# Kernel optimization log

Measured on AMD Instinct MI355X. Metric: run time of the kernel, lower is better.

Reference implementation:

```python
import jax, jax.numpy as jnp
import numpy as np

BS, D = 4096, 128
NUM_CLASSES = 512
K = 4          # opt.pk
MARGIN = 0.1   # opt.margin
NEG = -1e30    # sentinel for masked-out entries (finite to avoid inf*0 NaNs)


def setup_inputs() -> dict:
    key = jax.random.key(0)
    k1, k2 = jax.random.split(key)
    batch_reprs = jax.random.normal(k1, (BS, D), dtype=jnp.float32)
    batch_labels = jax.random.randint(k2, (BS,), 0, NUM_CLASSES, dtype=jnp.int64)
    return {"batch_reprs": batch_reprs, "batch_labels": batch_labels}


def _pairwise_dist(x, eps=1e-16):
    # Euclidean distance matrix, squared=False, with the usual zero-distance
    # masking trick for sqrt differentiability (as in the source repo's dist()).
    prod = x @ x.T                              # [B,B]
    sq = jnp.diagonal(prod)                     # [B]
    d2 = jnp.maximum(sq[:, None] + sq[None, :] - 2.0 * prod, 0.0)
    zero_mask = (d2 == 0.0).astype(x.dtype)
    d = jnp.sqrt(d2 + zero_mask * eps)
    return d * (1.0 - zero_mask)


def reference(batch_reprs, batch_labels):
    # class-match matrix: 1 where same class (includes self-match on diagonal)
    cls_match = (batch_labels[:, None] == batch_labels[None, :]).astype(jnp.float32)  # [B,B]

    sim_mat = -_pairwise_dist(batch_reprs)                      # use_similarity=False path
    simi_hat = sim_mat + (1.0 - cls_match) * MARGIN             # margin-shifted similarities

    # rank positions (1-based) under descending sort of simi_hat, per row
    orgp = jnp.argsort(-simi_hat, axis=1)                       # descending order indices
    rank = jnp.argsort(orgp, axis=1) + 1                        # [B,B] int ranks

    pos_nums = jnp.sum(cls_match, axis=1).astype(jnp.int32)     # n_+ per row (incl. self)
    ks = jnp.minimum(pos_nums, K + 1)                           # clamp(max=k+1)

    fp_mask = (cls_match < 1.0) & (rank <= ks[:, None])         # false positives in top-k
    fp_nums = jnp.sum(fp_mask, axis=1)                          # |N| per row, int
    fn_mask = (cls_match > 0.0) & (rank > ks[:, None])          # false negatives beyond k

    # per-row top-|N| of false-negative similarities, vectorized over rows
    fn_vals = jnp.where(fn_mask, simi_hat, NEG)
    fn_sorted = -jnp.sort(-fn_vals, axis=1)                     # descending
    col = jnp.arange(simi_hat.shape[1])[None, :]
    top_fn_sum = jnp.sum(jnp.where(col < fp_nums[:, None], fn_sorted, 0.0), axis=1)

    fp_sum = jnp.sum(jnp.where(fp_mask, simi_hat, 0.0), axis=1)

    # rows with fp_num == 0 contribute 0 in both terms, matching the python loop
    return jnp.sum(fp_sum - top_fn_sum)
```

## Files before the change

kernel.cpp:

```cpp
#include <hip/hip_runtime.h>
#include <math.h>

#define BS 4096
#define D 128
#define NC 512
#define NS 32
#define SC 128
#define MARGINF 0.1f
#define NEGV -1e30f
#define BIGD 1e30f
#define LSTR 12

typedef float f32x4 __attribute__((ext_vector_type(4)));
typedef short s16x8 __attribute__((ext_vector_type(8)));

__device__ __forceinline__ unsigned short f2bf(float f) {
    unsigned int u = __float_as_uint(f);
    unsigned int r = u + 0x7FFFu + ((u >> 16) & 1u);
    return (unsigned short)(r >> 16);
}

__device__ __forceinline__ void insV(float v, float (&V)[5]) {
    float w0 = fminf(V[0], v);
    float w1 = __builtin_amdgcn_fmed3f(V[0], V[1], v);
    float w2 = __builtin_amdgcn_fmed3f(V[1], V[2], v);
    float w3 = __builtin_amdgcn_fmed3f(V[2], V[3], v);
    float w4 = __builtin_amdgcn_fmed3f(V[3], V[4], v);
    V[0] = w0; V[1] = w1; V[2] = w2; V[3] = w3; V[4] = w4;
}

__device__ __forceinline__ void insDF(float v, int f, float (&V)[5], int (&F)[5]) {
#pragma unroll
    for (int t = 0; t < 5; ++t) {
        bool c = v > V[t];
        float tv = V[t]; int tf = F[t];
        V[t] = c ? v : tv; F[t] = c ? f : tf;
        v = c ? tv : v;    f = c ? tf : f;
    }
}

__global__ __launch_bounds__(256) void prep_kernel(
        const float* __restrict__ X, const int* __restrict__ labels,
        float* __restrict__ norms, int* __restrict__ counts,
        unsigned short* __restrict__ Xp) {
    __shared__ __align__(16) unsigned short sb[32 * 128];
    const int t = threadIdx.x, bx = blockIdx.x;
    const int row0 = bx * 32;

#pragma unroll
    for (int i = 0; i < 4; ++i) {
        int idx = i * 256 + t;
        int lr = idx >> 5, kq = idx & 31;
        float4 v = ((const float4*)X)[(size_t)row0 * 32 + idx];
        float acc = v.x * v.x + v.y * v.y + v.z * v.z + v.w * v.w;
#pragma unroll
        for (int off = 1; off < 32; off <<= 1) acc += __shfl_xor(acc, off);
        if (kq == 0) norms[row0 + lr] = acc;
        ushort4 hv = { f2bf(v.x), f2bf(v.y), f2bf(v.z), f2bf(v.w) };
        int chunk = (kq >> 1) ^ (lr & 7);
        *(ushort4*)((char*)sb + lr * 256 + (chunk << 4) + (kq & 1) * 8) = hv;
    }
    if (t < 32) atomicAdd(&counts[labels[row0 + t]], 1);
    __syncthreads();

#pragma unroll
    for (int i = 0; i < 2; ++i) {
        int u = i * 256 + t;
        int j = u >> 8, ug = u & 255;
        int ks = ug >> 6, l2 = ug & 63;
        int lr = j * 16 + (l2 & 15), q = l2 >> 4;
        int chunk = (ks * 4 + q) ^ (lr & 7);
        ulonglong2 d = *(const ulonglong2*)((const char*)sb + lr * 256 + (chunk << 4));
        *(ulonglong2*)((char*)Xp + (size_t)(bx * 2 + j) * 4096 + ks * 1024 + l2 * 16) = d;
    }
}

__global__ __launch_bounds__(256, 8) void main_kernel(
        const unsigned short* __restrict__ Xp, const int* __restrict__ labels,
        const float* __restrict__ norms, float* __restrict__ lists) {
    const int t = threadIdx.x, bx = blockIdx.x;
    const int slice = bx & (NS - 1);
    const int col0 = slice * SC;
    const int w = t >> 6, l = t & 63, rl = l & 15, q = l >> 4;
    const int gRow = (bx >> 5) * 4 + w;
    const int rowG = gRow * 16 + rl;
    const int lR = labels[rowG];
    const char* Pb = (const char*)Xp;

    s16x8 brow[4];
#pragma unroll
    for (int ks = 0; ks < 4; ++ks)
        brow[ks] = *(const s16x8*)(Pb + (size_t)gRow * 4096 + ks * 1024 + l * 16);

    f32x4 acc[8];
#pragma unroll
    for (int i = 0; i < 8; ++i) acc[i] = (f32x4){0.f, 0.f, 0.f, 0.f};

#pragma unroll
    for (int ks = 0; ks < 4; ++ks) {
        s16x8 af[8];
#pragma unroll
        for (int i = 0; i < 8; ++i)
            af[i] = *(const s16x8*)(Pb + (size_t)(slice * 8 + i) * 4096 + ks * 1024 + l * 16);
#pragma unroll
        for (int i = 0; i < 8; ++i)
            acc[i] = __builtin_amdgcn_mfma_f32_16x16x32_bf16(af[i], brow[ks], acc[i], 0, 0, 0);
    }

    float dV[5], sV[5];
#pragma unroll
    for (int i = 0; i < 5; ++i) { dV[i] = BIGD; sV[i] = BIGD; }

#pragma unroll
    for (int i = 0; i < 8; ++i) {
        f32x4 nc4 = *(const f32x4*)(norms + col0 + i * 16 + q * 4);
        int4  lc4 = *(const int4*)(labels + col0 + i * 16 + q * 4);
        int lcv[4] = {lc4.x, lc4.y, lc4.z, lc4.w};
#pragma unroll
        for (int e = 0; e < 4; ++e) {
            float v = fmaf(acc[i][e], -2.f, nc4[e]);
            bool same = (lcv[e] == lR);
            insV(same ? BIGD : v, dV);
            if (__any(same)) insV(same ? v : BIGD, sV);
        }
    }

#pragma unroll
    for (int off = 16; off <= 32; off <<= 1) {
        float bv[5];
#pragma unroll
        for (int i = 0; i < 5; ++i) bv[i] = __shfl_xor(dV[i], off);
#pragma unroll
        for (int i = 0; i < 5; ++i) insV(bv[i], dV);
#pragma unroll
        for (int i = 0; i < 5; ++i) bv[i] = __shfl_xor(sV[i], off);
#pragma unroll
        for (int i = 0; i < 5; ++i) insV(bv[i], sV);
    }

    if (q == 0) {
        float* Lp = lists + ((size_t)rowG * NS + slice) * LSTR;
        *(f32x4*)Lp       = (f32x4){dV[0], dV[1], dV[2], dV[3]};
        *(f32x4*)(Lp + 4) = (f32x4){dV[4], sV[4], 0.f, 0.f};
        *(f32x4*)(Lp + 8) = (f32x4){sV[0], sV[1], sV[2], sV[3]};
    }
}

__global__ __launch_bounds__(256) void merge_kernel(
        const float* __restrict__ lists, const int* __restrict__ counts,
        const int* __restrict__ labels, const float* __restrict__ norms,
        float* __restrict__ partials) {
    __shared__ float sh[256];
    const int t = threadIdx.x, bx = blockIdx.x;
    const int gid = bx * 256 + t;
    const int r = gid >> 3, part = gid & 7;
    const int half = part & 1, s8 = part >> 1;

    float V[5];
#pragma unroll
    for (int i = 0; i < 5; ++i) V[i] = BIGD;
#pragma unroll
    for (int s = 0; s < 8; ++s) {
        const float* rec = lists + (size_t)(r * NS + s8 * 8 + s) * LSTR + half * 8;
        f32x4 v4 = *(const f32x4*)rec;
        float v5 = rec[half ? -3 : 4];
        insV(v4.x, V); insV(v4.y, V); insV(v4.z, V); insV(v4.w, V); insV(v5, V);
    }
#pragma unroll
    for (int off = 2; off <= 4; off <<= 1) {
        float bv[5];
#pragma unroll
        for (int i = 0; i < 5; ++i) bv[i] = __shfl_xor(V[i], off);
#pragma unroll
        for (int i = 0; i < 5; ++i) insV(bv[i], V);
    }
    float oV[5];
#pragma unroll
    for (int i = 0; i < 5; ++i) oV[i] = __shfl_xor(V[i], 1);

    float res = 0.f;
    if (part == 0) {
        const float nR = norms[r];
        const int pos = counts[labels[r]];
        const int ks = (pos < 5) ? pos : 5;
        float dS[5], sS[5];
#pragma unroll
        for (int i = 0; i < 5; ++i) {
            float dv = V[i];  bool ok = dv < 1e29f;
            dS[i] = ok ? (-sqrtf(fmaxf(nR + dv, 0.f)) + MARGINF) : NEGV;
        }
#pragma unroll
        for (int i = 0; i < 5; ++i) {
            float sv = oV[i]; bool ok = sv < 1e29f;
            sS[i] = ok ? -sqrtf(fmaxf(nR + sv, 0.f)) : NEGV;
        }
        float mV[5]; int mF[5];
#pragma unroll
        for (int i = 0; i < 5; ++i) { mV[i] = dS[i]; mF[i] = 0; }
#pragma unroll
        for (int i = 0; i < 5; ++i) insDF(sS[i], 1, mV, mF);

        float fpsum = 0.f; int fpn = 0;
#pragma unroll
        for (int i = 0; i < 5; ++i)
            if (i < ks && mF[i] == 0) { fpsum += mV[i]; fpn++; }
        const int s0 = ks - fpn;
        float fnsum = 0.f;
#pragma unroll
        for (int i = 0; i < 5; ++i)
            if (i >= s0 && i < s0 + fpn) fnsum += sS[i];
        res = fpsum - fnsum;
    }
    sh[t] = res;
    __syncthreads();
    for (int s = 128; s > 0; s >>= 1) {
        if (t < s) sh[t] += sh[t + s];
        __syncthreads();
    }
    if (t == 0) partials[bx] = sh[0];
}

__global__ void reduce_kernel(const float* __restrict__ partials, float* __restrict__ out) {
    const int l = threadIdx.x;
    float v = partials[l] + partials[l + 64];
#pragma unroll
    for (int off = 1; off < 64; off <<= 1) v += __shfl_xor(v, off);
    if (l == 0) out[0] = v;
}

extern "C" void kernel_launch(void* const* d_in, const int* in_sizes, int n_in,
                              void* d_out, int out_size, void* d_ws, size_t ws_size,
                              hipStream_t stream) {
    const float* X      = (const float*)d_in[0];
    const int*   labels = (const int*)d_in[1];

    float* ws       = (float*)d_ws;
    float* norms    = ws;
    float* partials = ws + BS;
    int*   counts   = (int*)(ws + BS + 128);
    float* lists    = ws + BS + 128 + NC;
    unsigned short* Xp = (unsigned short*)(lists + (size_t)BS * NS * LSTR);

    hipMemsetAsync(counts, 0, NC * sizeof(int), stream);
    prep_kernel<<<BS / 32, 256, 0, stream>>>(X, labels, norms, counts, Xp);
    main_kernel<<<(BS / 64) * NS, 256, 0, stream>>>(Xp, labels, norms, lists);
    merge_kernel<<<(BS * 8) / 256, 256, 0, stream>>>(lists, counts, labels, norms, partials);
    reduce_kernel<<<1, 64, 0, stream>>>(partials, (float*)d_out);
}
```

Measured before the change: 45.00 us.

## Widen column slices, simplify merge, fold final reduction into merge via ticket

Each main_kernel block now walks 512 columns in four 128-column groups instead of handling a single 128-column slice. This cuts the grid fourfold and shrinks the per-row candidate list buffer from 32 slices to 8. The merge kernel now reads one 8-slice record per thread and merges both distance lists with shuffles. The separate reduce kernel is replaced by a last-block-done atomic ticket that sums the partials, removing one launch. The costs are fewer, longer blocks that may hide latency less well, and a serial 128-element sum run by a single thread.

```diff
diff --git a/kernel.cpp b/kernel.cpp
--- a/kernel.cpp
+++ b/kernel.cpp
@@ -4,8 +4,8 @@
 #define BS 4096
 #define D 128
 #define NC 512
-#define NS 32
-#define SC 128
+#define NS 8
+#define SC 512
 #define MARGINF 0.1f
 #define NEGV -1e30f
 #define BIGD 1e30f
@@ -82,7 +82,7 @@
     const int slice = bx & (NS - 1);
     const int col0 = slice * SC;
     const int w = t >> 6, l = t & 63, rl = l & 15, q = l >> 4;
-    const int gRow = (bx >> 5) * 4 + w;
+    const int gRow = (bx >> 3) * 4 + w;
     const int rowG = gRow * 16 + rl;
     const int lR = labels[rowG];
     const char* Pb = (const char*)Xp;
@@ -92,36 +92,39 @@
     for (int ks = 0; ks < 4; ++ks)
         brow[ks] = *(const s16x8*)(Pb + (size_t)gRow * 4096 + ks * 1024 + l * 16);
 
-    f32x4 acc[8];
-#pragma unroll
-    for (int i = 0; i < 8; ++i) acc[i] = (f32x4){0.f, 0.f, 0.f, 0.f};
-
-#pragma unroll
-    for (int ks = 0; ks < 4; ++ks) {
-        s16x8 af[8];
-#pragma unroll
-        for (int i = 0; i < 8; ++i)
-            af[i] = *(const s16x8*)(Pb + (size_t)(slice * 8 + i) * 4096 + ks * 1024 + l * 16);
-#pragma unroll
-        for (int i = 0; i < 8; ++i)
-            acc[i] = __builtin_amdgcn_mfma_f32_16x16x32_bf16(af[i], brow[ks], acc[i], 0, 0, 0);
-    }
-
     float dV[5], sV[5];
 #pragma unroll
     for (int i = 0; i < 5; ++i) { dV[i] = BIGD; sV[i] = BIGD; }
 
-#pragma unroll
-    for (int i = 0; i < 8; ++i) {
-        f32x4 nc4 = *(const f32x4*)(norms + col0 + i * 16 + q * 4);
-        int4  lc4 = *(const int4*)(labels + col0 + i * 16 + q * 4);
-        int lcv[4] = {lc4.x, lc4.y, lc4.z, lc4.w};
-#pragma unroll
-        for (int e = 0; e < 4; ++e) {
-            float v = fmaf(acc[i][e], -2.f, nc4[e]);
-            bool same = (lcv[e] == lR);
-            insV(same ? BIGD : v, dV);
-            if (__any(same)) insV(same ? v : BIGD, sV);
+#pragma unroll 1
+    for (int cg = 0; cg < 4; ++cg) {
+        f32x4 acc[8];
+#pragma unroll
+        for (int i = 0; i < 8; ++i) acc[i] = (f32x4){0.f, 0.f, 0.f, 0.f};
+
+#pragma unroll
+        for (int ks = 0; ks < 4; ++ks) {
+            s16x8 af[8];
+#pragma unroll
+            for (int i = 0; i < 8; ++i)
+                af[i] = *(const s16x8*)(Pb + (size_t)(slice * 32 + cg * 8 + i) * 4096 + ks * 1024 + l * 16);
+#pragma unroll
+            for (int i = 0; i < 8; ++i)
+                acc[i] = __builtin_amdgcn_mfma_f32_16x16x32_bf16(af[i], brow[ks], acc[i], 0, 0, 0);
+        }
+
+#pragma unroll
+        for (int i = 0; i < 8; ++i) {
+            f32x4 nc4 = *(const f32x4*)(norms + col0 + cg * 128 + i * 16 + q * 4);
+            int4  lc4 = *(const int4*)(labels + col0 + cg * 128 + i * 16 + q * 4);
+            int lcv[4] = {lc4.x, lc4.y, lc4.z, lc4.w};
+#pragma unroll
+            for (int e = 0; e < 4; ++e) {
+                float v = fmaf(acc[i][e], -2.f, nc4[e]);
+                bool same = (lcv[e] == lR);
+                insV(same ? BIGD : v, dV);
+                if (__any(same)) insV(same ? v : BIGD, sV);
+            }
         }
     }
 
@@ -149,34 +152,32 @@
 __global__ __launch_bounds__(256) void merge_kernel(
         const float* __restrict__ lists, const int* __restrict__ counts,
         const int* __restrict__ labels, const float* __restrict__ norms,
-        float* __restrict__ partials) {
+        float* __restrict__ partials, int* __restrict__ ticket,
+        float* __restrict__ out) {
     __shared__ float sh[256];
     const int t = threadIdx.x, bx = blockIdx.x;
     const int gid = bx * 256 + t;
     const int r = gid >> 3, part = gid & 7;
-    const int half = part & 1, s8 = part >> 1;
-
-    float V[5];
-#pragma unroll
-    for (int i = 0; i < 5; ++i) V[i] = BIGD;
-#pragma unroll
-    for (int s = 0; s < 8; ++s) {
-        const float* rec = lists + (size_t)(r * NS + s8 * 8 + s) * LSTR + half * 8;
-        f32x4 v4 = *(const f32x4*)rec;
-        float v5 = rec[half ? -3 : 4];
-        insV(v4.x, V); insV(v4.y, V); insV(v4.z, V); insV(v4.w, V); insV(v5, V);
-    }
-#pragma unroll
-    for (int off = 2; off <= 4; off <<= 1) {
+
+    const float* rec = lists + (size_t)(r * NS + part) * LSTR;
+    f32x4 a = *(const f32x4*)rec;
+    f32x4 b = *(const f32x4*)(rec + 4);
+    f32x4 c = *(const f32x4*)(rec + 8);
+    float dV[5] = {a.x, a.y, a.z, a.w, b.x};
+    float sV[5] = {c.x, c.y, c.z, c.w, b.y};
+
+#pragma unroll
+    for (int off = 1; off <= 4; off <<= 1) {
         float bv[5];
 #pragma unroll
-        for (int i = 0; i < 5; ++i) bv[i] = __shfl_xor(V[i], off);
-#pragma unroll
-        for (int i = 0; i < 5; ++i) insV(bv[i], V);
-    }
-    float oV[5];
-#pragma unroll
-    for (int i = 0; i < 5; ++i) oV[i] = __shfl_xor(V[i], 1);
+        for (int i = 0; i < 5; ++i) bv[i] = __shfl_xor(dV[i], off);
+#pragma unroll
+        for (int i = 0; i < 5; ++i) insV(bv[i], dV);
+#pragma unroll
+        for (int i = 0; i < 5; ++i) bv[i] = __shfl_xor(sV[i], off);
+#pragma unroll
+        for (int i = 0; i < 5; ++i) insV(bv[i], sV);
+    }
 
     float res = 0.f;
     if (part == 0) {
@@ -186,12 +187,12 @@
         float dS[5], sS[5];
 #pragma unroll
         for (int i = 0; i < 5; ++i) {
-            float dv = V[i];  bool ok = dv < 1e29f;
+            float dv = dV[i]; bool ok = dv < 1e29f;
             dS[i] = ok ? (-sqrtf(fmaxf(nR + dv, 0.f)) + MARGINF) : NEGV;
         }
 #pragma unroll
         for (int i = 0; i < 5; ++i) {
-            float sv = oV[i]; bool ok = sv < 1e29f;
+            float sv = sV[i]; bool ok = sv < 1e29f;
             sS[i] = ok ? -sqrtf(fmaxf(nR + sv, 0.f)) : NEGV;
         }
         float mV[5]; int mF[5];
@@ -217,15 +218,17 @@
         if (t < s) sh[t] += sh[t + s];
         __syncthreads();
     }
-    if (t == 0) partials[bx] = sh[0];
-}
-
-__global__ void reduce_kernel(const float* __restrict__ partials, float* __restrict__ out) {
-    const int l = threadIdx.x;
-    float v = partials[l] + partials[l + 64];
-#pragma unroll
-    for (int off = 1; off < 64; off <<= 1) v += __shfl_xor(v, off);
-    if (l == 0) out[0] = v;
+    if (t == 0) {
+        partials[bx] = sh[0];
+        __threadfence();
+        int old = atomicAdd(ticket, 1);
+        if (old == (int)gridDim.x - 1) {
+            __threadfence();
+            float s = 0.f;
+            for (int i = 0; i < (int)gridDim.x; ++i) s += partials[i];
+            out[0] = s;
+        }
+    }
 }
 
 extern "C" void kernel_launch(void* const* d_in, const int* in_sizes, int n_in,
@@ -238,12 +241,13 @@
     float* norms    = ws;
     float* partials = ws + BS;
     int*   counts   = (int*)(ws + BS + 128);
-    float* lists    = ws + BS + 128 + NC;
+    int*   ticket   = counts + NC;
+    float* lists    = ws + BS + 128 + NC + 16;
     unsigned short* Xp = (unsigned short*)(lists + (size_t)BS * NS * LSTR);
 
-    hipMemsetAsync(counts, 0, NC * sizeof(int), stream);
+    hipMemsetAsync(counts, 0, (NC + 16) * sizeof(int), stream);
     prep_kernel<<<BS / 32, 256, 0, stream>>>(X, labels, norms, counts, Xp);
     main_kernel<<<(BS / 64) * NS, 256, 0, stream>>>(Xp, labels, norms, lists);
-    merge_kernel<<<(BS * 8) / 256, 256, 0, stream>>>(lists, counts, labels, norms, partials);
-    reduce_kernel<<<1, 64, 0, stream>>>(partials, (float*)d_out);
-}
+    merge_kernel<<<(BS * 8) / 256, 256, 0, stream>>>(lists, counts, labels, norms,
+                                                     partials, ticket, (float*)d_out);
+}
```

Measured after the change: 66.78 us. +48.4%, slower.
